# Optimization experiments

Measured on AMD Instinct MI355X. Metric: run time of the kernel, lower is better.

## Reference

```python
import jax, jax.numpy as jnp
import numpy as np

N = 50000        # node_num
E = 1600000      # num edges
F_IN = 8
HID = 1000
R = 100          # robustness_length


def setup_inputs() -> dict:
    key = jax.random.key(0)
    ks = jax.random.split(key, 16)
    X = jax.random.normal(ks[0], (N, F_IN), dtype=jnp.float32)
    edge_index = jax.random.randint(ks[1], (2, E), 0, N, dtype=jnp.int64)
    s = 1.0 / np.sqrt(F_IN)
    # SAGEConv mean-aggr params (PyG: out = lin_l(aggr) + lin_r(x), lin_r has no bias)
    lin_l_w = jax.random.uniform(ks[2], (1, F_IN), jnp.float32, -s, s)
    lin_l_b = jax.random.uniform(ks[3], (1,), jnp.float32, -s, s)
    lin_r_w = jax.random.uniform(ks[4], (1, F_IN), jnp.float32, -s, s)
    # SAGEConv max-aggr params
    lin_l1_w = jax.random.uniform(ks[5], (1, F_IN), jnp.float32, -s, s)
    lin_l1_b = jax.random.uniform(ks[6], (1,), jnp.float32, -s, s)
    lin_r1_w = jax.random.uniform(ks[7], (1, F_IN), jnp.float32, -s, s)
    # MLP params
    s0 = 1.0 / np.sqrt(N)
    W0 = jax.random.uniform(ks[8], (HID, N), jnp.float32, -s0, s0)
    b0 = jax.random.uniform(ks[9], (HID,), jnp.float32, -s0, s0)
    s1 = 1.0 / np.sqrt(HID)
    W1 = jax.random.uniform(ks[10], (HID, HID), jnp.float32, -s1, s1)
    b1 = jax.random.uniform(ks[11], (HID,), jnp.float32, -s1, s1)
    W2 = jax.random.uniform(ks[12], (R, HID), jnp.float32, -s1, s1)
    b2 = jax.random.uniform(ks[13], (R,), jnp.float32, -s1, s1)
    return dict(X=X, edge_index=edge_index,
                lin_l_w=lin_l_w, lin_l_b=lin_l_b, lin_r_w=lin_r_w,
                lin_l1_w=lin_l1_w, lin_l1_b=lin_l1_b, lin_r1_w=lin_r1_w,
                W0=W0, b0=b0, W1=W1, b1=b1, W2=W2, b2=b2)


def reference(X, edge_index, lin_l_w, lin_l_b, lin_r_w,
              lin_l1_w, lin_l1_b, lin_r1_w,
              W0, b0, W1, b1, W2, b2):
    src, dst = edge_index[0], edge_index[1]
    msgs = X[src]  # [E, F_IN] gathered neighbor features
    cnt = jax.ops.segment_sum(jnp.ones((E,), jnp.float32), dst, num_segments=N)
    # mean aggregation (empty -> 0)
    agg_mean = jax.ops.segment_sum(msgs, dst, num_segments=N) / jnp.maximum(cnt, 1.0)[:, None]
    # max aggregation (empty -> 0, per PyG scatter-max fill)
    agg_max = jax.ops.segment_max(msgs, dst, num_segments=N)
    agg_max = jnp.where(cnt[:, None] > 0, agg_max, 0.0)
    # SAGEConv: lin_l(aggr) + lin_r(x)
    h_mean = jax.nn.relu(agg_mean @ lin_l_w.T + lin_l_b + X @ lin_r_w.T)   # [N,1]
    h_max = jax.nn.relu(agg_max @ lin_l1_w.T + lin_l1_b + X @ lin_r1_w.T)  # [N,1]
    x = (h_mean + h_max).reshape(-1)  # [N]
    X_embedding = x
    h = jax.nn.relu(W0 @ x + b0)
    h = jax.nn.relu(W1 @ h + b1)
    out = jax.nn.relu(W2 @ h + b2)
    return (X_embedding, out)
```

## Files before the change

### kernel.cpp

```cpp
#include <hip/hip_runtime.h>

#define N_NODES 50000
#define N_EDGES 1600000
#define F_IN 8
#define HID 1000
#define R_OUT 100

#define BSHIFT 6
#define NPB 64
#define NB 782
#define CAP_B 2400
#define CHUNK 4096
#define NBIN_BLOCKS ((N_EDGES + CHUNK - 1) / CHUNK)
#define NCHUNK0 25


__device__ __forceinline__ unsigned fkey(float f) {
    unsigned b = __float_as_uint(f);
    return (b & 0x80000000u) ? ~b : (b | 0x80000000u);
}
__device__ __forceinline__ float funkey(unsigned k) {
    unsigned b = (k & 0x80000000u) ? (k & 0x7fffffffu) : ~k;
    return __uint_as_float(b);
}

__global__ void init_ws(unsigned* __restrict__ p, int n) {
    int i = blockIdx.x * blockDim.x + threadIdx.x;
    if (i < n) p[i] = 0u;
}

__global__ void bin_kernel(const int* __restrict__ ei,
                           const float* __restrict__ X,
                           const float* __restrict__ wl,
                           int* __restrict__ cursor,
                           unsigned* __restrict__ binned,
                           int* __restrict__ ovf_cnt,
                           float* __restrict__ ovf_sum,
                           unsigned* __restrict__ ovf_max) {
    __shared__ int hist[NB];
    __shared__ int pos[NB];
    __shared__ int base[NB];
    int tid = threadIdx.x;
    int e0 = blockIdx.x * CHUNK;
    int e1 = e0 + CHUNK;
    if (e1 > N_EDGES) e1 = N_EDGES;

    for (int i = tid; i < NB; i += 256) { hist[i] = 0; pos[i] = 0; }
    __syncthreads();

    for (int e = e0 + tid; e < e1; e += 256) {
        int dst = ei[N_EDGES + e];
        atomicAdd(&hist[dst >> BSHIFT], 1);
    }
    __syncthreads();

    for (int b = tid; b < NB; b += 256) {
        int h = hist[b];
        base[b] = (h > 0) ? atomicAdd(&cursor[b], h) : 0;
    }
    __syncthreads();

    for (int e = e0 + tid; e < e1; e += 256) {
        int src = ei[e];
        int dst = ei[N_EDGES + e];
        int b = dst >> BSHIFT;
        int p = atomicAdd(&pos[b], 1);
        int gp = base[b] + p;
        if (gp < CAP_B) {
            binned[(size_t)b * CAP_B + gp] =
                (unsigned)src | ((unsigned)(dst & (NPB - 1)) << 16);
        } else {
            const float4* X4 = (const float4*)(X + src * F_IN);
            float4 a = X4[0], bb = X4[1];
            float f[8] = {a.x, a.y, a.z, a.w, bb.x, bb.y, bb.z, bb.w};
            float d = 0.f;
#pragma unroll
            for (int k = 0; k < 8; ++k) d += f[k] * wl[k];
            atomicAdd(&ovf_cnt[dst], 1);
            atomicAdd(&ovf_sum[dst], d);
            unsigned* mb = ovf_max + (size_t)dst * 8;
#pragma unroll
            for (int k = 0; k < 8; ++k) atomicMax(&mb[k], fkey(f[k]));
        }
    }
}

__global__ void agg_kernel(const int* __restrict__ cursor,
                           const unsigned* __restrict__ binned,
                           const int* __restrict__ ovf_cnt,
                           const float* __restrict__ ovf_sum,
                           const unsigned* __restrict__ ovf_max,
                           const float* __restrict__ X,
                           const float* __restrict__ lin_l_w,
                           const float* __restrict__ lin_l_b,
                           const float* __restrict__ lin_r_w,
                           const float* __restrict__ lin_l1_w,
                           const float* __restrict__ lin_l1_b,
                           const float* __restrict__ lin_r1_w,
                           float* __restrict__ xemb) {
    __shared__ unsigned lds[NPB * 10];
    float* sdot = (float*)lds;
    unsigned* scnt = lds + NPB;
    unsigned* smax = lds + 2 * NPB;

    int b = blockIdx.x;
    int tid = threadIdx.x;

    for (int i = tid; i < NPB * 10; i += 256) lds[i] = 0u;
    __syncthreads();

    float wl[8];
#pragma unroll
    for (int k = 0; k < 8; ++k) wl[k] = lin_l_w[k];

    int n = cursor[b];
    if (n > CAP_B) n = CAP_B;
    const unsigned* list = binned + (size_t)b * CAP_B;
    for (int j = tid; j < n; j += 256) {
        unsigned p = list[j];
        int src = p & 0xFFFF;
        int dlow = p >> 16;
        const float4* X4 = (const float4*)(X + src * F_IN);
        float4 a = X4[0], bb = X4[1];
        float f[8] = {a.x, a.y, a.z, a.w, bb.x, bb.y, bb.z, bb.w};
        float d = 0.f;
#pragma unroll
        for (int k = 0; k < 8; ++k) d += f[k] * wl[k];
        atomicAdd(&sdot[dlow], d);
        atomicAdd(&scnt[dlow], 1u);
#pragma unroll
        for (int k = 0; k < 8; ++k) atomicMax(&smax[k * NPB + dlow], fkey(f[k]));
    }
    __syncthreads();

    if (tid < NPB) {
        int node = b * NPB + tid;
        if (node < N_NODES) {
            int oc = ovf_cnt[node];
            int total = (int)scnt[tid] + oc;
            float sumdot = sdot[tid] + ovf_sum[node];
            float mx[8];
#pragma unroll
            for (int k = 0; k < 8; ++k) mx[k] = funkey(smax[k * NPB + tid]);
            if (oc > 0) {
                const unsigned* mb = ovf_max + (size_t)node * 8;
#pragma unroll
                for (int k = 0; k < 8; ++k) mx[k] = fmaxf(mx[k], funkey(mb[k]));
            }
            float c = (float)total;
            float mean_dot = sumdot / fmaxf(c, 1.0f);
            const float4* X4 = (const float4*)(X + node * F_IN);
            float4 a = X4[0], bb = X4[1];
            float f[8] = {a.x, a.y, a.z, a.w, bb.x, bb.y, bb.z, bb.w};
            float dr = 0.f, dr1 = 0.f, dmax = 0.f;
            bool nonempty = (total > 0);
#pragma unroll
            for (int k = 0; k < 8; ++k) {
                float m = nonempty ? mx[k] : 0.0f;
                dmax += m * lin_l1_w[k];
                dr   += f[k] * lin_r_w[k];
                dr1  += f[k] * lin_r1_w[k];
            }
            float hm = fmaxf(mean_dot + lin_l_b[0] + dr, 0.f);
            float hx = fmaxf(dmax + lin_l1_b[0] + dr1, 0.f);
            xemb[node] = hm + hx;
        }
    }
}


template <int BLOCK, int NCHUNK>
__global__ void gemv_partial(const float* __restrict__ W,
                             const float* __restrict__ x,
                             float* __restrict__ part, int cols) {
    int row = blockIdx.x;
    int c = blockIdx.y;
    int chunk = cols / NCHUNK;
    const float4* W4 = (const float4*)(W + (size_t)row * cols + (size_t)c * chunk);
    const float4* x4 = (const float4*)(x + c * chunk);
    int n4 = chunk >> 2;
    float s = 0.f;
    for (int j = threadIdx.x; j < n4; j += BLOCK) {
        float4 w = W4[j], xx = x4[j];
        s += w.x * xx.x + w.y * xx.y + w.z * xx.z + w.w * xx.w;
    }
#pragma unroll
    for (int off = 32; off > 0; off >>= 1) s += __shfl_down(s, off, 64);
    __shared__ float red[BLOCK / 64];
    int t = threadIdx.x;
    if ((t & 63) == 0) red[t >> 6] = s;
    __syncthreads();
    if (t == 0) {
        float tot = 0.f;
#pragma unroll
        for (int w = 0; w < BLOCK / 64; ++w) tot += red[w];
        part[row * NCHUNK + c] = tot;
    }
}

template <int NCHUNK>
__global__ void gemv_finalize(const float* __restrict__ part,
                              const float* __restrict__ bias,
                              float* __restrict__ y, int rows) {
    int r = blockIdx.x * blockDim.x + threadIdx.x;
    if (r >= rows) return;
    float s = 0.f;
#pragma unroll
    for (int c = 0; c < NCHUNK; ++c) s += part[r * NCHUNK + c];
    y[r] = fmaxf(s + bias[r], 0.f);
}

template <int BLOCK>
__global__ void gemv_relu(const float* __restrict__ W,
                          const float* __restrict__ x,
                          const float* __restrict__ bias,
                          float* __restrict__ y, int cols) {
    int row = blockIdx.x;
    const float4* W4 = (const float4*)(W + (size_t)row * cols);
    const float4* x4 = (const float4*)x;
    int n4 = cols >> 2;
    float s = 0.f;
    for (int j = threadIdx.x; j < n4; j += BLOCK) {
        float4 w = W4[j], xx = x4[j];
        s += w.x * xx.x + w.y * xx.y + w.z * xx.z + w.w * xx.w;
    }
#pragma unroll
    for (int off = 32; off > 0; off >>= 1) s += __shfl_down(s, off, 64);
    __shared__ float red[BLOCK / 64];
    int t = threadIdx.x;
    if ((t & 63) == 0) red[t >> 6] = s;
    __syncthreads();
    if (t == 0) {
        float tot = 0.f;
#pragma unroll
        for (int w = 0; w < BLOCK / 64; ++w) tot += red[w];
        y[row] = fmaxf(tot + bias[row], 0.f);
    }
}


__global__ void edge_kernel_fb(const int* __restrict__ ei,
                               const float* __restrict__ X,
                               const float* __restrict__ wl,
                               float* __restrict__ sumw,
                               float* __restrict__ cnt,
                               unsigned* __restrict__ maxb) {
    int e = blockIdx.x * blockDim.x + threadIdx.x;
    if (e >= N_EDGES) return;
    int src = ei[e];
    int dst = ei[N_EDGES + e];
    const float4* X4 = (const float4*)(X + src * F_IN);
    float4 a = X4[0], b = X4[1];
    float f[8] = {a.x, a.y, a.z, a.w, b.x, b.y, b.z, b.w};
    float d = 0.f;
#pragma unroll
    for (int k = 0; k < 8; ++k) d += f[k] * wl[k];
    atomicAdd(&sumw[dst], d);
    atomicAdd(&cnt[dst], 1.0f);
    unsigned* mb = maxb + (size_t)dst * 8;
#pragma unroll
    for (int k = 0; k < 8; ++k) atomicMax(&mb[k], fkey(f[k]));
}

__global__ void node_kernel_fb(const float* __restrict__ X,
                               const float* __restrict__ sumw,
                               const float* __restrict__ cnt,
                               const unsigned* __restrict__ maxb,
                               const float* __restrict__ lin_l_b,
                               const float* __restrict__ lin_r_w,
                               const float* __restrict__ lin_l1_w,
                               const float* __restrict__ lin_l1_b,
                               const float* __restrict__ lin_r1_w,
                               float* __restrict__ xout) {
    int i = blockIdx.x * blockDim.x + threadIdx.x;
    if (i >= N_NODES) return;
    float c = cnt[i];
    float mean_dot = sumw[i] / fmaxf(c, 1.0f);
    const float4* X4 = (const float4*)(X + i * F_IN);
    float4 a = X4[0], b = X4[1];
    float f[8] = {a.x, a.y, a.z, a.w, b.x, b.y, b.z, b.w};
    const uint4* M4 = (const uint4*)(maxb + (size_t)i * 8);
    uint4 m0 = M4[0], m1 = M4[1];
    unsigned mk[8] = {m0.x, m0.y, m0.z, m0.w, m1.x, m1.y, m1.z, m1.w};
    float dr = 0.f, dr1 = 0.f, dmax = 0.f;
    bool nonempty = (c > 0.f);
#pragma unroll
    for (int k = 0; k < 8; ++k) {
        float mxv = nonempty ? funkey(mk[k]) : 0.0f;
        dmax += mxv * lin_l1_w[k];
        dr   += f[k] * lin_r_w[k];
        dr1  += f[k] * lin_r1_w[k];
    }
    float hm = fmaxf(mean_dot + lin_l_b[0] + dr, 0.f);
    float hx = fmaxf(dmax + lin_l1_b[0] + dr1, 0.f);
    xout[i] = hm + hx;
}


extern "C" void kernel_launch(void* const* d_in, const int* in_sizes, int n_in,
                              void* d_out, int out_size, void* d_ws, size_t ws_size,
                              hipStream_t stream) {
    const float* X        = (const float*)d_in[0];
    const int*   ei       = (const int*)d_in[1];
    const float* lin_l_w  = (const float*)d_in[2];
    const float* lin_l_b  = (const float*)d_in[3];
    const float* lin_r_w  = (const float*)d_in[4];
    const float* lin_l1_w = (const float*)d_in[5];
    const float* lin_l1_b = (const float*)d_in[6];
    const float* lin_r1_w = (const float*)d_in[7];
    const float* W0       = (const float*)d_in[8];
    const float* b0       = (const float*)d_in[9];
    const float* W1       = (const float*)d_in[10];
    const float* b1       = (const float*)d_in[11];
    const float* W2       = (const float*)d_in[12];
    const float* b2       = (const float*)d_in[13];

    float* xemb = (float*)d_out;
    float* out2 = xemb + N_NODES;

    const size_t zero_words = (size_t)NB + (size_t)N_NODES * 10;
    const size_t need_words = zero_words + (size_t)NB * CAP_B
                              + (size_t)HID * NCHUNK0 + 2 * HID;
    if (ws_size >= need_words * 4) {
        int*      cursor  = (int*)d_ws;
        int*      ovf_cnt = cursor + NB;
        float*    ovf_sum = (float*)(ovf_cnt + N_NODES);
        unsigned* ovf_max = (unsigned*)(ovf_sum + N_NODES);
        unsigned* binned  = ovf_max + (size_t)N_NODES * 8;
        float*    part0   = (float*)(binned + (size_t)NB * CAP_B);
        float*    h0      = part0 + HID * NCHUNK0;
        float*    h1      = h0 + HID;

        hipLaunchKernelGGL(init_ws, dim3(((int)zero_words + 255) / 256), dim3(256), 0, stream,
                           (unsigned*)d_ws, (int)zero_words);
        hipLaunchKernelGGL(bin_kernel, dim3(NBIN_BLOCKS), dim3(256), 0, stream,
                           ei, X, lin_l_w, cursor, binned, ovf_cnt, ovf_sum, ovf_max);
        hipLaunchKernelGGL(agg_kernel, dim3(NB), dim3(256), 0, stream,
                           cursor, binned, ovf_cnt, ovf_sum, ovf_max, X,
                           lin_l_w, lin_l_b, lin_r_w, lin_l1_w, lin_l1_b, lin_r1_w, xemb);

        hipLaunchKernelGGL((gemv_partial<256, NCHUNK0>), dim3(HID, NCHUNK0), dim3(256), 0, stream,
                           W0, xemb, part0, N_NODES);
        hipLaunchKernelGGL(gemv_finalize<NCHUNK0>, dim3((HID + 255) / 256), dim3(256), 0, stream,
                           part0, b0, h0, HID);
        hipLaunchKernelGGL(gemv_relu<256>, dim3(HID), dim3(256), 0, stream,
                           W1, h0, b1, h1, HID);
        hipLaunchKernelGGL(gemv_relu<256>, dim3(R_OUT), dim3(256), 0, stream,
                           W2, h1, b2, out2, HID);
    } else {
        float*    sumw = (float*)d_ws;
        float*    cntf = sumw + N_NODES;
        unsigned* maxb = (unsigned*)(cntf + N_NODES);
        float*    h0   = (float*)(maxb + (size_t)N_NODES * 8);
        float*    h1   = h0 + HID;

        int zw = N_NODES * 10;
        hipLaunchKernelGGL(init_ws, dim3((zw + 255) / 256), dim3(256), 0, stream,
                           (unsigned*)d_ws, zw);
        hipLaunchKernelGGL(edge_kernel_fb, dim3((N_EDGES + 255) / 256), dim3(256), 0, stream,
                           ei, X, lin_l_w, sumw, cntf, maxb);
        hipLaunchKernelGGL(node_kernel_fb, dim3((N_NODES + 255) / 256), dim3(256), 0, stream,
                           X, sumw, cntf, maxb, lin_l_b, lin_r_w, lin_l1_w, lin_l1_b,
                           lin_r1_w, xemb);
        hipLaunchKernelGGL(gemv_relu<256>, dim3(HID), dim3(256), 0, stream,
                           W0, xemb, b0, h0, N_NODES);
        hipLaunchKernelGGL(gemv_relu<256>, dim3(HID), dim3(256), 0, stream,
                           W1, h0, b1, h1, HID);
        hipLaunchKernelGGL(gemv_relu<256>, dim3(R_OUT), dim3(256), 0, stream,
                           W2, h1, b2, out2, HID);
    }
}
```

Baseline: 380.0 us.

## Sort bins by destination in LDS and reduce with registers instead of atomics

```diff
diff --git a/kernel.cpp b/kernel.cpp
--- a/kernel.cpp
+++ b/kernel.cpp
@@ -37,6 +37,8 @@
                            int* __restrict__ ovf_cnt,
                            float* __restrict__ ovf_sum,
                            unsigned* __restrict__ ovf_max) {
+    __shared__ unsigned sEntry[CHUNK];
+    __shared__ unsigned short sBucket[CHUNK];
     __shared__ int hist[NB];
     __shared__ int pos[NB];
     __shared__ int base[NB];
@@ -44,13 +46,18 @@
     int e0 = blockIdx.x * CHUNK;
     int e1 = e0 + CHUNK;
     if (e1 > N_EDGES) e1 = N_EDGES;
+    int ne = e1 - e0;
 
     for (int i = tid; i < NB; i += 256) { hist[i] = 0; pos[i] = 0; }
     __syncthreads();
 
-    for (int e = e0 + tid; e < e1; e += 256) {
-        int dst = ei[N_EDGES + e];
-        atomicAdd(&hist[dst >> BSHIFT], 1);
+    for (int j = tid; j < ne; j += 256) {
+        int src = ei[e0 + j];
+        int dst = ei[N_EDGES + e0 + j];
+        int b = dst >> BSHIFT;
+        sEntry[j] = (unsigned)src | ((unsigned)(dst & (NPB - 1)) << 16);
+        sBucket[j] = (unsigned short)b;
+        atomicAdd(&hist[b], 1);
     }
     __syncthreads();
 
@@ -60,16 +67,16 @@
     }
     __syncthreads();
 
-    for (int e = e0 + tid; e < e1; e += 256) {
-        int src = ei[e];
-        int dst = ei[N_EDGES + e];
-        int b = dst >> BSHIFT;
+    for (int j = tid; j < ne; j += 256) {
+        unsigned entry = sEntry[j];
+        int b = sBucket[j];
         int p = atomicAdd(&pos[b], 1);
         int gp = base[b] + p;
         if (gp < CAP_B) {
-            binned[(size_t)b * CAP_B + gp] =
-                (unsigned)src | ((unsigned)(dst & (NPB - 1)) << 16);
+            binned[(size_t)b * CAP_B + gp] = entry;
         } else {
+            int src = entry & 0xFFFF;
+            int dst = b * NPB + (int)(entry >> 16);
             const float4* X4 = (const float4*)(X + src * F_IN);
             float4 a = X4[0], bb = X4[1];
             float f[8] = {a.x, a.y, a.z, a.w, bb.x, bb.y, bb.z, bb.w};
@@ -98,57 +105,88 @@
                            const float* __restrict__ lin_l1_b,
                            const float* __restrict__ lin_r1_w,
                            float* __restrict__ xemb) {
-    __shared__ unsigned lds[NPB * 10];
-    float* sdot = (float*)lds;
-    unsigned* scnt = lds + NPB;
-    unsigned* smax = lds + 2 * NPB;
+    __shared__ unsigned sEntry[CAP_B];
+    __shared__ unsigned sSorted[CAP_B];
+    __shared__ int sCnt[NPB];
+    __shared__ int sOff[NPB];
+    __shared__ int sPos[NPB];
 
     int b = blockIdx.x;
     int tid = threadIdx.x;
-
-    for (int i = tid; i < NPB * 10; i += 256) lds[i] = 0u;
-    __syncthreads();
-
-    float wl[8];
-#pragma unroll
-    for (int k = 0; k < 8; ++k) wl[k] = lin_l_w[k];
-
     int n = cursor[b];
     if (n > CAP_B) n = CAP_B;
-    const unsigned* list = binned + (size_t)b * CAP_B;
+
+    if (tid < NPB) { sCnt[tid] = 0; sPos[tid] = 0; }
+    __syncthreads();
+
     for (int j = tid; j < n; j += 256) {
-        unsigned p = list[j];
-        int src = p & 0xFFFF;
-        int dlow = p >> 16;
+        unsigned e = binned[(size_t)b * CAP_B + j];
+        sEntry[j] = e;
+        atomicAdd(&sCnt[e >> 16], 1);
+    }
+    __syncthreads();
+
+    if (tid == 0) {
+        int run = 0;
+#pragma unroll
+        for (int i = 0; i < NPB; ++i) { sOff[i] = run; run += sCnt[i]; }
+    }
+    __syncthreads();
+
+    for (int j = tid; j < n; j += 256) {
+        unsigned e = sEntry[j];
+        int d = e >> 16;
+        int p = atomicAdd(&sPos[d], 1);
+        sSorted[sOff[d] + p] = e;
+    }
+    __syncthreads();
+
+    int nl = tid >> 2;
+    int r = tid & 3;
+    int beg = sOff[nl];
+    int cnt = sCnt[nl];
+
+    float wl[8];
+#pragma unroll
+    for (int k = 0; k < 8; ++k) wl[k] = lin_l_w[k];
+
+    float sumdot = 0.f;
+    float mx[8];
+#pragma unroll
+    for (int k = 0; k < 8; ++k) mx[k] = -INFINITY;
+
+    for (int j = beg + r; j < beg + cnt; j += 4) {
+        int src = sSorted[j] & 0xFFFF;
         const float4* X4 = (const float4*)(X + src * F_IN);
         float4 a = X4[0], bb = X4[1];
         float f[8] = {a.x, a.y, a.z, a.w, bb.x, bb.y, bb.z, bb.w};
         float d = 0.f;
 #pragma unroll
         for (int k = 0; k < 8; ++k) d += f[k] * wl[k];
-        atomicAdd(&sdot[dlow], d);
-        atomicAdd(&scnt[dlow], 1u);
-#pragma unroll
-        for (int k = 0; k < 8; ++k) atomicMax(&smax[k * NPB + dlow], fkey(f[k]));
-    }
-    __syncthreads();
-
-    if (tid < NPB) {
-        int node = b * NPB + tid;
+        sumdot += d;
+#pragma unroll
+        for (int k = 0; k < 8; ++k) mx[k] = fmaxf(mx[k], f[k]);
+    }
+#pragma unroll
+    for (int m = 1; m <= 2; m <<= 1) {
+        sumdot += __shfl_xor(sumdot, m, 4);
+#pragma unroll
+        for (int k = 0; k < 8; ++k) mx[k] = fmaxf(mx[k], __shfl_xor(mx[k], m, 4));
+    }
+
+    if (r == 0) {
+        int node = b * NPB + nl;
         if (node < N_NODES) {
             int oc = ovf_cnt[node];
-            int total = (int)scnt[tid] + oc;
-            float sumdot = sdot[tid] + ovf_sum[node];
-            float mx[8];
-#pragma unroll
-            for (int k = 0; k < 8; ++k) mx[k] = funkey(smax[k * NPB + tid]);
+            int total = cnt + oc;
+            float sd = sumdot + ovf_sum[node];
             if (oc > 0) {
                 const unsigned* mb = ovf_max + (size_t)node * 8;
 #pragma unroll
                 for (int k = 0; k < 8; ++k) mx[k] = fmaxf(mx[k], funkey(mb[k]));
             }
             float c = (float)total;
-            float mean_dot = sumdot / fmaxf(c, 1.0f);
+            float mean_dot = sd / fmaxf(c, 1.0f);
             const float4* X4 = (const float4*)(X + node * F_IN);
             float4 a = X4[0], bb = X4[1];
             float f[8] = {a.x, a.y, a.z, a.w, bb.x, bb.y, bb.z, bb.w};
```

Result: faster. 359.6 us (-5.4%).
